# Kernel optimization log

Measured on AMD Instinct MI355X. Metric: run time of the kernel, lower is better.

Reference implementation:

```python
import jax, jax.numpy as jnp
import numpy as np

N = 50000          # nodes
E = 800000         # edges (COO)
IN_CH = 128
H1, H2, OUT = 200, 100, 2   # 100*out, 50*out, out with out_channels=2
EPS = 1e-12
DROP_P = 0.1


def setup_inputs() -> dict:
    key = jax.random.key(0)
    ks = jax.random.split(key, 6)
    x = jax.random.normal(ks[0], (N, IN_CH), dtype=jnp.float32)
    edge_index = jax.random.randint(ks[1], (2, E), 0, N)
    W1 = jax.random.normal(ks[2], (IN_CH, H1), dtype=jnp.float32) / np.sqrt(IN_CH)
    W2 = jax.random.normal(ks[3], (H1, H2), dtype=jnp.float32) / np.sqrt(H1)
    W3 = jax.random.normal(ks[4], (H2, OUT), dtype=jnp.float32) / np.sqrt(H2)
    beta1 = jnp.float32(1.0)
    beta2 = jnp.float32(1.0)
    beta3 = jnp.float32(1.0)
    return dict(x=x, edge_index=edge_index, W1=W1, W2=W2, W3=W3,
                beta1=beta1, beta2=beta2, beta3=beta3)


def _agnn_layer(x, W, beta, src, dst):
    # project in -> out channels, then AGNN cosine-attention propagation
    h = x @ W                                               # [N, D]
    hn = h / jnp.maximum(jnp.linalg.norm(h, axis=-1, keepdims=True), EPS)
    a = beta * jnp.sum(hn[src] * hn[dst], axis=-1)          # [E'] edge logits
    amax = jax.ops.segment_max(a, dst, num_segments=N)      # stable segment softmax
    amax = jnp.where(jnp.isfinite(amax), amax, 0.0)
    e = jnp.exp(a - amax[dst])
    denom = jax.ops.segment_sum(e, dst, num_segments=N)
    alpha = e / jnp.maximum(denom[dst], EPS)
    return jax.ops.segment_sum(h[src] * alpha[:, None], dst, num_segments=N)


def _dropout(k, x, p=DROP_P):
    keep = jax.random.bernoulli(k, 1.0 - p, x.shape)
    return jnp.where(keep, x / (1.0 - p), 0.0)


def reference(x, edge_index, W1, W2, W3, beta1, beta2, beta3):
    src, dst = edge_index[0], edge_index[1]
    loop = jnp.arange(N)                                    # self-loops (AGNNConv default)
    src = jnp.concatenate([src, loop])
    dst = jnp.concatenate([dst, loop])
    k1, k2 = jax.random.split(jax.random.key(42))
    h = jax.nn.relu(_agnn_layer(x, W1, beta1, src, dst))
    h = _dropout(k1, h)
    h = jax.nn.relu(_agnn_layer(h, W2, beta2, src, dst))
    h = _dropout(k2, h)
    h = jax.nn.relu(_agnn_layer(h, W3, beta3, src, dst))
    return h
```

## Files before the change

### kernel.cpp

```cpp
#include <hip/hip_runtime.h>
#include <hip/hip_bf16.h>

#define NN 50000
#define NE 800000
#define EPSN 1e-12f


#define H_OFF    0ull
#define A_OFF    40000000ull
#define H3_OFF   80000000ull
#define RINV_OFF 80400000ull
#define OFFS_OFF 80600000ull
#define DEG_OFF  80800016ull
#define CURS_OFF 81000016ull
#define ESRC_OFF 81200016ull
#define CHNK_OFF 84600016ull

__host__ __device__ inline void tf20(unsigned k0, unsigned k1, unsigned& x0, unsigned& x1) {
  unsigned ks2 = k0 ^ k1 ^ 0x1BD11BDAu;
  x0 += k0; x1 += k1;
#define TFR(r) { x0 += x1; x1 = ((x1 << (r)) | (x1 >> (32 - (r)))) ^ x0; }
  TFR(13) TFR(15) TFR(26) TFR(6)
  x0 += k1;  x1 += ks2 + 1u;
  TFR(17) TFR(29) TFR(16) TFR(24)
  x0 += ks2; x1 += k0 + 2u;
  TFR(13) TFR(15) TFR(26) TFR(6)
  x0 += k0;  x1 += k1 + 3u;
  TFR(17) TFR(29) TFR(16) TFR(24)
  x0 += k1;  x1 += ks2 + 4u;
  TFR(13) TFR(15) TFR(26) TFR(6)
  x0 += ks2; x1 += k0 + 5u;
#undef TFR
}

__device__ __forceinline__ float dropf(float val, unsigned k0, unsigned k1, unsigned i) {
  unsigned x0 = 0u, x1 = i;
  tf20(k0, k1, x0, x1);
  unsigned bits = x0 ^ x1;
  float u = __uint_as_float((bits >> 9) | 0x3F800000u) - 1.0f;
  return (u < 0.9f) ? val * (1.0f / 0.9f) : 0.0f;
}

__device__ __forceinline__ float wave_sum(float x) {
  x += __shfl_xor(x, 32); x += __shfl_xor(x, 16); x += __shfl_xor(x, 8);
  x += __shfl_xor(x, 4);  x += __shfl_xor(x, 2);  x += __shfl_xor(x, 1);
  return x;
}

template<int K, int KT, int NLP, int N>
__device__ __forceinline__ void gemm_core4(float* __restrict__ As, float* __restrict__ Ws,
                                           const float* __restrict__ A,
                                           const float* __restrict__ W,
                                           float* __restrict__ H,
                                           float* __restrict__ RINV, int M, int row0) {
  static_assert(NLP % 64 == 0 && KT % 4 == 0, "layout");
  constexpr int KTP = KT + 1, NV = N / 4, NC = NLP / 64, PD4 = NLP / 4 - NV;
  const float4* A4 = (const float4*)A;
  const float4* W4 = (const float4*)W;
  const float4* Ws4 = (const float4*)Ws;

  int t = threadIdx.x, rgrp = t >> 4, cg = t & 15;
  float acc[4][NC * 4];
#pragma unroll
  for (int rr = 0; rr < 4; rr++)
#pragma unroll
    for (int j = 0; j < NC * 4; j++) acc[rr][j] = 0.f;

  for (int k0 = 0; k0 < K; k0 += KT) {
    __syncthreads();
    for (int idx = t; idx < 64 * (KT / 4); idx += 256) {
      int r = idx / (KT / 4), cq = idx - r * (KT / 4);
      int gr = row0 + r;
      float4 v = (gr < M) ? A4[(size_t)gr * (K / 4) + (k0 / 4) + cq]
                          : make_float4(0.f, 0.f, 0.f, 0.f);
      float* dst = &As[r * KTP + cq * 4];
      dst[0] = v.x; dst[1] = v.y; dst[2] = v.z; dst[3] = v.w;
    }
    for (int idx = t; idx < KT * NV; idx += 256) {
      int kk = idx / NV, cq = idx - kk * NV;
      *(float4*)&Ws[kk * NLP + cq * 4] = W4[(size_t)(k0 + kk) * NV + cq];
    }
    for (int idx = t; idx < KT * PD4; idx += 256) {
      int kk = idx / PD4, pq = idx - kk * PD4;
      *(float4*)&Ws[kk * NLP + N + pq * 4] = make_float4(0.f, 0.f, 0.f, 0.f);
    }
    __syncthreads();
#pragma unroll
    for (int kk = 0; kk < KT; kk++) {
      float a[4];
#pragma unroll
      for (int rr = 0; rr < 4; rr++) a[rr] = As[(rgrp * 4 + rr) * KTP + kk];
#pragma unroll
      for (int q = 0; q < NC; q++) {
        float4 wv = Ws4[kk * (NLP / 4) + cg + 16 * q];
#pragma unroll
        for (int rr = 0; rr < 4; rr++) {
          acc[rr][q * 4 + 0] = fmaf(a[rr], wv.x, acc[rr][q * 4 + 0]);
          acc[rr][q * 4 + 1] = fmaf(a[rr], wv.y, acc[rr][q * 4 + 1]);
          acc[rr][q * 4 + 2] = fmaf(a[rr], wv.z, acc[rr][q * 4 + 2]);
          acc[rr][q * 4 + 3] = fmaf(a[rr], wv.w, acc[rr][q * 4 + 3]);
        }
      }
    }
  }

  int r0 = row0 + rgrp * 4;
#pragma unroll
  for (int rr = 0; rr < 4; rr++) {
    int gr = r0 + rr;
    float ss = 0.f;
#pragma unroll
    for (int q = 0; q < NC; q++) {
#pragma unroll
      for (int j = 0; j < 4; j++) {
        float v = acc[rr][q * 4 + j];
        ss += v * v;
        int c = 4 * (cg + 16 * q) + j;
        if (gr < M && c < N) H[(size_t)gr * N + c] = v;
      }
    }
    ss += __shfl_xor(ss, 1); ss += __shfl_xor(ss, 2);
    ss += __shfl_xor(ss, 4); ss += __shfl_xor(ss, 8);
    if (cg == 0 && gr < M) RINV[gr] = 1.0f / fmaxf(sqrtf(ss), EPSN);
  }
}

__global__ __launch_bounds__(256, 4) void gemm1_hist_kernel(
    const float* __restrict__ X, const float* __restrict__ W1,
    float* __restrict__ H, float* __restrict__ RINV,
    const int* __restrict__ EI, int* __restrict__ DEG) {
  __shared__ float As[64 * 17];
  __shared__ float Ws[16 * 256];
  int bid = blockIdx.x;
  if (bid < 782) {
    gemm_core4<128, 16, 256, 200>(As, Ws, X, W1, H, RINV, NN, bid * 64);
  } else {
    for (int e = (bid - 782) * 256 + threadIdx.x; e < NE; e += 242 * 256)
      atomicAdd(&DEG[EI[NE + e]], 1);
  }
}

__global__ __launch_bounds__(256, 4) void gemm2_kernel(const float* __restrict__ A,
                                                       const float* __restrict__ W,
                                                       float* __restrict__ H,
                                                       float* __restrict__ RINV, int M) {
  __shared__ float As[64 * 41];
  __shared__ float Ws[40 * 128];
  gemm_core4<200, 40, 128, 100>(As, Ws, A, W, H, RINV, M, blockIdx.x * 64);
}

__global__ __launch_bounds__(256) void csr_scan1_kernel(const int* __restrict__ deg,
                                                        int* __restrict__ offs,
                                                        int* __restrict__ chunk) {
  __shared__ int lds[8];
  int t = threadIdx.x;
  int base = blockIdx.x * 1024 + t * 4;
  int d[4];
#pragma unroll
  for (int j = 0; j < 4; j++) d[j] = (base + j < NN) ? deg[base + j] : 0;
  int ts = d[0] + d[1] + d[2] + d[3];
  int lane = t & 63, wave = t >> 6;
  int inc = ts;
#pragma unroll
  for (int sh = 1; sh < 64; sh <<= 1) { int u = __shfl_up(inc, sh); if (lane >= sh) inc += u; }
  if (lane == 63) lds[wave] = inc;
  __syncthreads();
  if (t == 0) { int s = 0; for (int w = 0; w < 4; w++) { int x = lds[w]; lds[w] = s; s += x; } lds[4] = s; }
  __syncthreads();
  int p = lds[wave] + inc - ts;
#pragma unroll
  for (int j = 0; j < 4; j++) { if (base + j < NN) offs[base + j] = p; p += d[j]; }
  if (t == 255) chunk[blockIdx.x] = lds[4];
}

__global__ __launch_bounds__(64) void csr_scan2_kernel(int* __restrict__ chunk) {
  int t = threadIdx.x;
  int v = (t < 49) ? chunk[t] : 0;
  int inc = v;
#pragma unroll
  for (int sh = 1; sh < 64; sh <<= 1) { int u = __shfl_up(inc, sh); if (t >= sh) inc += u; }
  if (t < 49) chunk[t] = inc - v;
}

__global__ __launch_bounds__(256) void csr_scan3_kernel(int* __restrict__ offs,
                                                        const int* __restrict__ chunk,
                                                        int* __restrict__ curs) {
  int i = blockIdx.x * 256 + threadIdx.x;
  if (i < NN) {
    int val = offs[i] + chunk[i >> 10];
    offs[i] = val;
    curs[i] = val;
  }
  if (i == 0) offs[NN] = NE;
}

__global__ __launch_bounds__(256) void csr_scatter_kernel(const int* __restrict__ ei,
                                                          int* __restrict__ curs,
                                                          int* __restrict__ esrc) {
  int e = blockIdx.x * 256 + threadIdx.x;
  if (e >= NE) return;
  int s = ei[e], d = ei[NE + e];
  int pos = atomicAdd(&curs[d], 1);
  esrc[pos] = s;
}

template<int D, int VEC, bool DROP>
__device__ __forceinline__ void attn_body(const float* __restrict__ H,
                                          const float* __restrict__ RINV,
                                          const int* __restrict__ OFFS,
                                          const int* __restrict__ ESRC,
                                          const float* __restrict__ BETA,
                                          float* __restrict__ OUT,
                                          unsigned k0, unsigned k1) {
  constexpr int NL = D / VEC;
  int v = blockIdx.x * 4 + (threadIdx.x >> 6);
  int lane = threadIdx.x & 63;
  bool act = lane < NL;
  float beta = BETA[0];
  float bd = beta * RINV[v];
  int e0 = OFFS[v], e1 = OFFS[v + 1];

  float wself = __expf(beta);
  float s = wself;
  float hd[VEC], acc[VEC];
  if (act) {
    const float* hrow = H + (size_t)v * D + lane * VEC;
    if (VEC == 4) { float4 tv = *(const float4*)hrow; hd[0] = tv.x; hd[1] = tv.y; hd[2] = tv.z; hd[3] = tv.w; }
    else          { float2 tv = *(const float2*)hrow; hd[0] = tv.x; hd[1] = tv.y; }
#pragma unroll
    for (int j = 0; j < VEC; j++) acc[j] = wself * hd[j];
  }

  int idx = e0;
  for (; idx + 4 <= e1; idx += 4) {
    int   u[4];
    float r[4], dt[4], hs[4][VEC];
#pragma unroll
    for (int m = 0; m < 4; m++) u[m] = ESRC[idx + m];
#pragma unroll
    for (int m = 0; m < 4; m++) r[m] = RINV[u[m]];
    float dd[4] = {0.f, 0.f, 0.f, 0.f};
    if (act) {
#pragma unroll
      for (int m = 0; m < 4; m++) {
        const float* p = H + (size_t)u[m] * D + lane * VEC;
        if (VEC == 4) { float4 a = *(const float4*)p; hs[m][0] = a.x; hs[m][1] = a.y; hs[m][2] = a.z; hs[m][3] = a.w; }
        else          { float2 a = *(const float2*)p; hs[m][0] = a.x; hs[m][1] = a.y; }
      }
#pragma unroll
      for (int m = 0; m < 4; m++)
#pragma unroll
        for (int j = 0; j < VEC; j++) dd[m] = fmaf(hd[j], hs[m][j], dd[m]);
    }
#pragma unroll
    for (int m = 0; m < 4; m++) dt[m] = wave_sum(dd[m]);
    float w[4];
#pragma unroll
    for (int m = 0; m < 4; m++) { w[m] = __expf(bd * dt[m] * r[m]); s += w[m]; }
    if (act) {
#pragma unroll
      for (int m = 0; m < 4; m++)
#pragma unroll
        for (int j = 0; j < VEC; j++) acc[j] = fmaf(w[m], hs[m][j], acc[j]);
    }
  }
  for (; idx < e1; ++idx) {
    int u0 = ESRC[idx];
    float r0 = RINV[u0];
    float h0[VEC];
    float ddt = 0.f;
    if (act) {
      const float* p0 = H + (size_t)u0 * D + lane * VEC;
      if (VEC == 4) { float4 a = *(const float4*)p0; h0[0] = a.x; h0[1] = a.y; h0[2] = a.z; h0[3] = a.w; }
      else          { float2 a = *(const float2*)p0; h0[0] = a.x; h0[1] = a.y; }
#pragma unroll
      for (int j = 0; j < VEC; j++) ddt = fmaf(hd[j], h0[j], ddt);
    }
    ddt = wave_sum(ddt);
    float w0 = __expf(bd * ddt * r0);
    s += w0;
    if (act) {
#pragma unroll
      for (int j = 0; j < VEC; j++) acc[j] = fmaf(w0, h0[j], acc[j]);
    }
  }

  float rs = 1.0f / fmaxf(s, EPSN);
  if (act) {
    float o[VEC];
#pragma unroll
    for (int j = 0; j < VEC; j++) {
      float val = acc[j] * rs;
      val = (val <= 0.0f) ? 0.0f : val;
      if (DROP) val = dropf(val, k0, k1, (unsigned)(v * D + lane * VEC + j));
      o[j] = val;
    }
    float* orow = OUT + (size_t)v * D + lane * VEC;
    if (VEC == 4) *(float4*)orow = make_float4(o[0], o[1], o[2], o[3]);
    else          *(float2*)orow = make_float2(o[0], o[1]);
  }
}

__global__ __launch_bounds__(256) void attn1_kernel(const float* H, const float* RINV,
                                                    const int* OFFS, const int* ESRC,
                                                    const float* BETA, float* OUT,
                                                    unsigned k0, unsigned k1) {
  attn_body<200, 4, true>(H, RINV, OFFS, ESRC, BETA, OUT, k0, k1);
}

__global__ __launch_bounds__(256) void attn2_proj_kernel(
    const float* __restrict__ H, const float* __restrict__ RINV,
    const int* __restrict__ OFFS, const int* __restrict__ ESRC,
    const float* __restrict__ BETA, const float* __restrict__ W3,
    float* __restrict__ H3, float* __restrict__ RINV3,
    unsigned k0, unsigned k1) {
  constexpr int D = 100, VEC = 2, NL = 50;
  int v = blockIdx.x * 4 + (threadIdx.x >> 6);
  int lane = threadIdx.x & 63;
  bool act = lane < NL;
  float beta = BETA[0];
  float bd = beta * RINV[v];
  int e0 = OFFS[v], e1 = OFFS[v + 1];

  float4 w3v = make_float4(0.f, 0.f, 0.f, 0.f);
  if (act) w3v = *(const float4*)&W3[4 * lane];

  float wself = __expf(beta);
  float s = wself;
  float hd[VEC], acc[VEC];
  if (act) {
    const float* hrow = H + (size_t)v * D + lane * VEC;
    float2 tv = *(const float2*)hrow; hd[0] = tv.x; hd[1] = tv.y;
#pragma unroll
    for (int j = 0; j < VEC; j++) acc[j] = wself * hd[j];
  }

  int idx = e0;
  for (; idx + 4 <= e1; idx += 4) {
    int   u[4];
    float r[4], dt[4], hs[4][VEC];
#pragma unroll
    for (int m = 0; m < 4; m++) u[m] = ESRC[idx + m];
#pragma unroll
    for (int m = 0; m < 4; m++) r[m] = RINV[u[m]];
    float dd[4] = {0.f, 0.f, 0.f, 0.f};
    if (act) {
#pragma unroll
      for (int m = 0; m < 4; m++) {
        const float* p = H + (size_t)u[m] * D + lane * VEC;
        float2 a = *(const float2*)p; hs[m][0] = a.x; hs[m][1] = a.y;
      }
#pragma unroll
      for (int m = 0; m < 4; m++)
#pragma unroll
        for (int j = 0; j < VEC; j++) dd[m] = fmaf(hd[j], hs[m][j], dd[m]);
    }
#pragma unroll
    for (int m = 0; m < 4; m++) dt[m] = wave_sum(dd[m]);
    float w[4];
#pragma unroll
    for (int m = 0; m < 4; m++) { w[m] = __expf(bd * dt[m] * r[m]); s += w[m]; }
    if (act) {
#pragma unroll
      for (int m = 0; m < 4; m++)
#pragma unroll
        for (int j = 0; j < VEC; j++) acc[j] = fmaf(w[m], hs[m][j], acc[j]);
    }
  }
  for (; idx < e1; ++idx) {
    int u0 = ESRC[idx];
    float r0 = RINV[u0];
    float h0[VEC];
    float ddt = 0.f;
    if (act) {
      const float* p0 = H + (size_t)u0 * D + lane * VEC;
      float2 a = *(const float2*)p0; h0[0] = a.x; h0[1] = a.y;
#pragma unroll
      for (int j = 0; j < VEC; j++) ddt = fmaf(hd[j], h0[j], ddt);
    }
    ddt = wave_sum(ddt);
    float w0 = __expf(bd * ddt * r0);
    s += w0;
    if (act) {
#pragma unroll
      for (int j = 0; j < VEC; j++) acc[j] = fmaf(w0, h0[j], acc[j]);
    }
  }

  float rs = 1.0f / fmaxf(s, EPSN);
  float p0 = 0.f, p1 = 0.f;
  if (act) {
    float o[VEC];
#pragma unroll
    for (int j = 0; j < VEC; j++) {
      float val = acc[j] * rs;
      val = (val <= 0.0f) ? 0.0f : val;
      val = dropf(val, k0, k1, (unsigned)(v * D + lane * VEC + j));
      o[j] = val;
    }
    p0 = o[0] * w3v.x + o[1] * w3v.z;
    p1 = o[0] * w3v.y + o[1] * w3v.w;
  }
  p0 = wave_sum(p0);
  p1 = wave_sum(p1);
  if (lane == 0) {
    H3[2 * v] = p0; H3[2 * v + 1] = p1;
    RINV3[v] = 1.0f / fmaxf(sqrtf(p0 * p0 + p1 * p1), EPSN);
  }
}

__global__ __launch_bounds__(256) void attn3_kernel(const float* __restrict__ H3,
                                                    const float* __restrict__ RINV3,
                                                    const int* __restrict__ OFFS,
                                                    const int* __restrict__ ESRC,
                                                    const float* __restrict__ BETA,
                                                    float* __restrict__ out) {
  int v = blockIdx.x * 4 + (threadIdx.x >> 6);
  int lane = threadIdx.x & 63;
  float beta = BETA[0];
  float bd = beta * RINV3[v];
  float h0 = H3[2 * v], h1 = H3[2 * v + 1];
  int e0 = OFFS[v], e1 = OFFS[v + 1];
  float s = 0.f, a0 = 0.f, a1 = 0.f;
  for (int idx = e0 + lane; idx < e1; idx += 64) {
    int u = ESRC[idx];
    float s0 = H3[2 * u], s1 = H3[2 * u + 1];
    float w = __expf(bd * (h0 * s0 + h1 * s1) * RINV3[u]);
    s += w; a0 = fmaf(w, s0, a0); a1 = fmaf(w, s1, a1);
  }
  s = wave_sum(s); a0 = wave_sum(a0); a1 = wave_sum(a1);
  if (lane == 0) {
    float wself = __expf(beta);
    s += wself; a0 = fmaf(wself, h0, a0); a1 = fmaf(wself, h1, a1);
    float rs = 1.0f / fmaxf(s, EPSN);
    float o0 = a0 * rs, o1 = a1 * rs;
    out[2 * v]     = (o0 <= 0.0f) ? 0.0f : o0;
    out[2 * v + 1] = (o1 <= 0.0f) ? 0.0f : o1;
  }
}

extern "C" void kernel_launch(void* const* d_in, const int* in_sizes, int n_in,
                              void* d_out, int out_size, void* d_ws, size_t ws_size,
                              hipStream_t stream) {
  const float* X  = (const float*)d_in[0];
  const int*   EI = (const int*)d_in[1];
  const float* W1 = (const float*)d_in[2];
  const float* W2 = (const float*)d_in[3];
  const float* W3 = (const float*)d_in[4];
  const float* B1 = (const float*)d_in[5];
  const float* B2 = (const float*)d_in[6];
  const float* B3 = (const float*)d_in[7];

  char* ws = (char*)d_ws;
  float* H     = (float*)(ws + H_OFF);
  float* A     = (float*)(ws + A_OFF);
  float* H3    = (float*)(ws + H3_OFF);
  float* RINV  = (float*)(ws + RINV_OFF);
  int* OFFS    = (int*)(ws + OFFS_OFF);
  int* DEG     = (int*)(ws + DEG_OFF);
  int* CURS    = (int*)(ws + CURS_OFF);
  float* RINV3 = (float*)(ws + CURS_OFF);
  int* ESRC    = (int*)(ws + ESRC_OFF);
  int* CHNK    = (int*)(ws + CHNK_OFF);

  unsigned k1a = 0u, k1b = 0u; tf20(0u, 42u, k1a, k1b);
  unsigned k2a = 0u, k2b = 1u; tf20(0u, 42u, k2a, k2b);

  hipMemsetAsync(DEG, 0, NN * sizeof(int), stream);

  gemm1_hist_kernel<<<1024, 256, 0, stream>>>(X, W1, H, RINV, EI, DEG);
  csr_scan1_kernel<<<49, 256, 0, stream>>>(DEG, OFFS, CHNK);
  csr_scan2_kernel<<<1, 64, 0, stream>>>(CHNK);
  csr_scan3_kernel<<<196, 256, 0, stream>>>(OFFS, CHNK, CURS);
  csr_scatter_kernel<<<(NE + 255) / 256, 256, 0, stream>>>(EI, CURS, ESRC);

  const int gb = (NN + 63) / 64;
  const int ab = NN / 4;

  attn1_kernel<<<ab, 256, 0, stream>>>(H, RINV, OFFS, ESRC, B1, A, k1a, k1b);
  gemm2_kernel<<<gb, 256, 0, stream>>>(A, W2, H, RINV, NN);
  attn2_proj_kernel<<<ab, 256, 0, stream>>>(H, RINV, OFFS, ESRC, B2, W3, H3, RINV3, k2a, k2b);
  attn3_kernel<<<ab, 256, 0, stream>>>(H3, RINV3, OFFS, ESRC, B3, (float*)d_out);
}
```

Before: 464.7 us.

## Schedule attention waves over nodes sorted by descending in-degree

Adds a counting sort of nodes by in-degree (histogram, scan, scatter into a permutation), and the three attention kernels now take their node through this permutation. High-degree nodes run first, which is meant to cut load imbalance and the long tail of waves. The inner loops also drop the per-lane active predicate and instead zero-fill inactive lanes. This costs three small extra kernels and a memset, and block-level locality between neighbouring node ids is lost.

New measurement: 751.7 us. +61.8%, slower.

```diff
diff --git a/kernel.cpp b/kernel.cpp
--- a/kernel.cpp
+++ b/kernel.cpp
@@ -14,6 +14,7 @@
 #define DEG_OFF  80800016ull
 #define CURS_OFF 81000016ull
 #define ESRC_OFF 81200016ull
+#define VPRM_OFF 84400016ull
 #define CHNK_OFF 84600016ull
 
 __host__ __device__ inline void tf20(unsigned k0, unsigned k1, unsigned& x0, unsigned& x1) {
@@ -204,32 +205,73 @@
   esrc[pos] = s;
 }
 
+__global__ __launch_bounds__(256) void perm_hist_kernel(const int* __restrict__ deg,
+                                                        int* __restrict__ pbkt) {
+  int v = blockIdx.x * 256 + threadIdx.x;
+  if (v >= NN) return;
+  int b = 511 - min(deg[v], 511);
+  atomicAdd(&pbkt[b], 1);
+}
+
+__global__ __launch_bounds__(256) void perm_scan_kernel(const int* __restrict__ pbkt,
+                                                        int* __restrict__ pcur) {
+  __shared__ int lds[8];
+  int t = threadIdx.x;
+  int b0 = pbkt[2 * t], b1 = pbkt[2 * t + 1];
+  int ts = b0 + b1;
+  int lane = t & 63, wave = t >> 6;
+  int inc = ts;
+#pragma unroll
+  for (int sh = 1; sh < 64; sh <<= 1) { int u = __shfl_up(inc, sh); if (lane >= sh) inc += u; }
+  if (lane == 63) lds[wave] = inc;
+  __syncthreads();
+  if (t == 0) { int s = 0; for (int w = 0; w < 4; w++) { int x = lds[w]; lds[w] = s; s += x; } }
+  __syncthreads();
+  int p = lds[wave] + inc - ts;
+  pcur[2 * t] = p;
+  pcur[2 * t + 1] = p + b0;
+}
+
+__global__ __launch_bounds__(256) void perm_scat_kernel(const int* __restrict__ deg,
+                                                        int* __restrict__ pcur,
+                                                        int* __restrict__ vperm) {
+  int v = blockIdx.x * 256 + threadIdx.x;
+  if (v >= NN) return;
+  int b = 511 - min(deg[v], 511);
+  int pos = atomicAdd(&pcur[b], 1);
+  vperm[pos] = v;
+}
+
 template<int D, int VEC, bool DROP>
 __device__ __forceinline__ void attn_body(const float* __restrict__ H,
                                           const float* __restrict__ RINV,
                                           const int* __restrict__ OFFS,
                                           const int* __restrict__ ESRC,
+                                          const int* __restrict__ VPERM,
                                           const float* __restrict__ BETA,
                                           float* __restrict__ OUT,
                                           unsigned k0, unsigned k1) {
   constexpr int NL = D / VEC;
-  int v = blockIdx.x * 4 + (threadIdx.x >> 6);
+  int v = VPERM[blockIdx.x * 4 + (threadIdx.x >> 6)];
   int lane = threadIdx.x & 63;
   bool act = lane < NL;
+  const float* hrow = H + (size_t)v * D + lane * VEC;
+  float hd[VEC];
+#pragma unroll
+  for (int j = 0; j < VEC; j++) hd[j] = 0.f;
+  if (act) {
+    if (VEC == 4) { float4 tv = *(const float4*)hrow; hd[0] = tv.x; hd[1] = tv.y; hd[2] = tv.z; hd[3] = tv.w; }
+    else          { float2 tv = *(const float2*)hrow; hd[0] = tv.x; hd[1] = tv.y; }
+  }
   float beta = BETA[0];
   float bd = beta * RINV[v];
   int e0 = OFFS[v], e1 = OFFS[v + 1];
 
   float wself = __expf(beta);
   float s = wself;
-  float hd[VEC], acc[VEC];
-  if (act) {
-    const float* hrow = H + (size_t)v * D + lane * VEC;
-    if (VEC == 4) { float4 tv = *(const float4*)hrow; hd[0] = tv.x; hd[1] = tv.y; hd[2] = tv.z; hd[3] = tv.w; }
-    else          { float2 tv = *(const float2*)hrow; hd[0] = tv.x; hd[1] = tv.y; }
-#pragma unroll
-    for (int j = 0; j < VEC; j++) acc[j] = wself * hd[j];
-  }
+  float acc[VEC];
+#pragma unroll
+  for (int j = 0; j < VEC; j++) acc[j] = wself * hd[j];
 
   int idx = e0;
   for (; idx + 4 <= e1; idx += 4) {
@@ -239,50 +281,50 @@
     for (int m = 0; m < 4; m++) u[m] = ESRC[idx + m];
 #pragma unroll
     for (int m = 0; m < 4; m++) r[m] = RINV[u[m]];
-    float dd[4] = {0.f, 0.f, 0.f, 0.f};
-    if (act) {
-#pragma unroll
-      for (int m = 0; m < 4; m++) {
-        const float* p = H + (size_t)u[m] * D + lane * VEC;
+#pragma unroll
+    for (int m = 0; m < 4; m++) {
+      const float* p = H + (size_t)u[m] * D + lane * VEC;
+#pragma unroll
+      for (int j = 0; j < VEC; j++) hs[m][j] = 0.f;
+      if (act) {
         if (VEC == 4) { float4 a = *(const float4*)p; hs[m][0] = a.x; hs[m][1] = a.y; hs[m][2] = a.z; hs[m][3] = a.w; }
         else          { float2 a = *(const float2*)p; hs[m][0] = a.x; hs[m][1] = a.y; }
       }
-#pragma unroll
-      for (int m = 0; m < 4; m++)
-#pragma unroll
-        for (int j = 0; j < VEC; j++) dd[m] = fmaf(hd[j], hs[m][j], dd[m]);
-    }
-#pragma unroll
-    for (int m = 0; m < 4; m++) dt[m] = wave_sum(dd[m]);
-    float w[4];
-#pragma unroll
-    for (int m = 0; m < 4; m++) { w[m] = __expf(bd * dt[m] * r[m]); s += w[m]; }
-    if (act) {
-#pragma unroll
-      for (int m = 0; m < 4; m++)
-#pragma unroll
-        for (int j = 0; j < VEC; j++) acc[j] = fmaf(w[m], hs[m][j], acc[j]);
+    }
+#pragma unroll
+    for (int m = 0; m < 4; m++) {
+      float d = 0.f;
+#pragma unroll
+      for (int j = 0; j < VEC; j++) d = fmaf(hd[j], hs[m][j], d);
+      dt[m] = wave_sum(d);
+    }
+#pragma unroll
+    for (int m = 0; m < 4; m++) {
+      float w = __expf(bd * dt[m] * r[m]);
+      s += w;
+#pragma unroll
+      for (int j = 0; j < VEC; j++) acc[j] = fmaf(w, hs[m][j], acc[j]);
     }
   }
   for (; idx < e1; ++idx) {
     int u0 = ESRC[idx];
     float r0 = RINV[u0];
+    const float* p0 = H + (size_t)u0 * D + lane * VEC;
     float h0[VEC];
-    float ddt = 0.f;
+#pragma unroll
+    for (int j = 0; j < VEC; j++) h0[j] = 0.f;
     if (act) {
-      const float* p0 = H + (size_t)u0 * D + lane * VEC;
       if (VEC == 4) { float4 a = *(const float4*)p0; h0[0] = a.x; h0[1] = a.y; h0[2] = a.z; h0[3] = a.w; }
       else          { float2 a = *(const float2*)p0; h0[0] = a.x; h0[1] = a.y; }
-#pragma unroll
-      for (int j = 0; j < VEC; j++) ddt = fmaf(hd[j], h0[j], ddt);
-    }
-    ddt = wave_sum(ddt);
-    float w0 = __expf(bd * ddt * r0);
+    }
+    float d0 = 0.f;
+#pragma unroll
+    for (int j = 0; j < VEC; j++) d0 = fmaf(hd[j], h0[j], d0);
+    d0 = wave_sum(d0);
+    float w0 = __expf(bd * d0 * r0);
     s += w0;
-    if (act) {
-#pragma unroll
-      for (int j = 0; j < VEC; j++) acc[j] = fmaf(w0, h0[j], acc[j]);
-    }
+#pragma unroll
+    for (int j = 0; j < VEC; j++) acc[j] = fmaf(w0, h0[j], acc[j]);
   }
 
   float rs = 1.0f / fmaxf(s, EPSN);
@@ -303,37 +345,39 @@
 
 __global__ __launch_bounds__(256) void attn1_kernel(const float* H, const float* RINV,
                                                     const int* OFFS, const int* ESRC,
+                                                    const int* VPERM,
                                                     const float* BETA, float* OUT,
                                                     unsigned k0, unsigned k1) {
-  attn_body<200, 4, true>(H, RINV, OFFS, ESRC, BETA, OUT, k0, k1);
+  attn_body<200, 4, true>(H, RINV, OFFS, ESRC, VPERM, BETA, OUT, k0, k1);
 }
 
 __global__ __launch_bounds__(256) void attn2_proj_kernel(
     const float* __restrict__ H, const float* __restrict__ RINV,
     const int* __restrict__ OFFS, const int* __restrict__ ESRC,
+    const int* __restrict__ VPERM,
     const float* __restrict__ BETA, const float* __restrict__ W3,
     float* __restrict__ H3, float* __restrict__ RINV3,
     unsigned k0, unsigned k1) {
   constexpr int D = 100, VEC = 2, NL = 50;
-  int v = blockIdx.x * 4 + (threadIdx.x >> 6);
+  int v = VPERM[blockIdx.x * 4 + (threadIdx.x >> 6)];
   int lane = threadIdx.x & 63;
   bool act = lane < NL;
+  const float* hrow = H + (size_t)v * D + lane * VEC;
+  float hd[VEC];
+  hd[0] = 0.f; hd[1] = 0.f;
+  float4 w3v = make_float4(0.f, 0.f, 0.f, 0.f);
+  if (act) {
+    float2 tv = *(const float2*)hrow; hd[0] = tv.x; hd[1] = tv.y;
+    w3v = *(const float4*)&W3[4 * lane];
+  }
   float beta = BETA[0];
   float bd = beta * RINV[v];
   int e0 = OFFS[v], e1 = OFFS[v + 1];
 
-  float4 w3v = make_float4(0.f, 0.f, 0.f, 0.f);
-  if (act) w3v = *(const float4*)&W3[4 * lane];
-
   float wself = __expf(beta);
   float s = wself;
-  float hd[VEC], acc[VEC];
-  if (act) {
-    const float* hrow = H + (size_t)v * D + lane * VEC;
-    float2 tv = *(const float2*)hrow; hd[0] = tv.x; hd[1] = tv.y;
-#pragma unroll
-    for (int j = 0; j < VEC; j++) acc[j] = wself * hd[j];
-  }
+  float acc[VEC];
+  acc[0] = wself * hd[0]; acc[1] = wself * hd[1];
 
   int idx = e0;
   for (; idx + 4 <= e1; idx += 4) {
@@ -343,63 +387,54 @@
     for (int m = 0; m < 4; m++) u[m] = ESRC[idx + m];
 #pragma unroll
     for (int m = 0; m < 4; m++) r[m] = RINV[u[m]];
-    float dd[4] = {0.f, 0.f, 0.f, 0.f};
-    if (act) {
-#pragma unroll
-      for (int m = 0; m < 4; m++) {
-        const float* p = H + (size_t)u[m] * D + lane * VEC;
-        float2 a = *(const float2*)p; hs[m][0] = a.x; hs[m][1] = a.y;
-      }
-#pragma unroll
-      for (int m = 0; m < 4; m++)
-#pragma unroll
-        for (int j = 0; j < VEC; j++) dd[m] = fmaf(hd[j], hs[m][j], dd[m]);
-    }
-#pragma unroll
-    for (int m = 0; m < 4; m++) dt[m] = wave_sum(dd[m]);
-    float w[4];
-#pragma unroll
-    for (int m = 0; m < 4; m++) { w[m] = __expf(bd * dt[m] * r[m]); s += w[m]; }
-    if (act) {
-#pragma unroll
-      for (int m = 0; m < 4; m++)
-#pragma unroll
-        for (int j = 0; j < VEC; j++) acc[j] = fmaf(w[m], hs[m][j], acc[j]);
+#pragma unroll
+    for (int m = 0; m < 4; m++) {
+      const float* p = H + (size_t)u[m] * D + lane * VEC;
+      hs[m][0] = 0.f; hs[m][1] = 0.f;
+      if (act) { float2 a = *(const float2*)p; hs[m][0] = a.x; hs[m][1] = a.y; }
+    }
+#pragma unroll
+    for (int m = 0; m < 4; m++) {
+      float d = 0.f;
+#pragma unroll
+      for (int j = 0; j < VEC; j++) d = fmaf(hd[j], hs[m][j], d);
+      dt[m] = wave_sum(d);
+    }
+#pragma unroll
+    for (int m = 0; m < 4; m++) {
+      float w = __expf(bd * dt[m] * r[m]);
+      s += w;
+#pragma unroll
+      for (int j = 0; j < VEC; j++) acc[j] = fmaf(w, hs[m][j], acc[j]);
     }
   }
   for (; idx < e1; ++idx) {
     int u0 = ESRC[idx];
     float r0 = RINV[u0];
+    const float* p0 = H + (size_t)u0 * D + lane * VEC;
     float h0[VEC];
-    float ddt = 0.f;
-    if (act) {
-      const float* p0 = H + (size_t)u0 * D + lane * VEC;
-      float2 a = *(const float2*)p0; h0[0] = a.x; h0[1] = a.y;
-#pragma unroll
-      for (int j = 0; j < VEC; j++) ddt = fmaf(hd[j], h0[j], ddt);
-    }
-    ddt = wave_sum(ddt);
-    float w0 = __expf(bd * ddt * r0);
+    h0[0] = 0.f; h0[1] = 0.f;
+    if (act) { float2 a = *(const float2*)p0; h0[0] = a.x; h0[1] = a.y; }
+    float d0 = 0.f;
+#pragma unroll
+    for (int j = 0; j < VEC; j++) d0 = fmaf(hd[j], h0[j], d0);
+    d0 = wave_sum(d0);
+    float w0 = __expf(bd * d0 * r0);
     s += w0;
-    if (act) {
-#pragma unroll
-      for (int j = 0; j < VEC; j++) acc[j] = fmaf(w0, h0[j], acc[j]);
-    }
+#pragma unroll
+    for (int j = 0; j < VEC; j++) acc[j] = fmaf(w0, h0[j], acc[j]);
   }
 
   float rs = 1.0f / fmaxf(s, EPSN);
   float p0 = 0.f, p1 = 0.f;
   if (act) {
-    float o[VEC];
-#pragma unroll
-    for (int j = 0; j < VEC; j++) {
-      float val = acc[j] * rs;
-      val = (val <= 0.0f) ? 0.0f : val;
-      val = dropf(val, k0, k1, (unsigned)(v * D + lane * VEC + j));
-      o[j] = val;
-    }
-    p0 = o[0] * w3v.x + o[1] * w3v.z;
-    p1 = o[0] * w3v.y + o[1] * w3v.w;
+    float o0 = acc[0] * rs, o1 = acc[1] * rs;
+    o0 = (o0 <= 0.0f) ? 0.0f : o0;
+    o1 = (o1 <= 0.0f) ? 0.0f : o1;
+    o0 = dropf(o0, k0, k1, (unsigned)(v * D + lane * VEC));
+    o1 = dropf(o1, k0, k1, (unsigned)(v * D + lane * VEC + 1));
+    p0 = o0 * w3v.x + o1 * w3v.z;
+    p1 = o0 * w3v.y + o1 * w3v.w;
   }
   p0 = wave_sum(p0);
   p1 = wave_sum(p1);
@@ -413,9 +448,10 @@
                                                     const float* __restrict__ RINV3,
                                                     const int* __restrict__ OFFS,
                                                     const int* __restrict__ ESRC,
+                                                    const int* __restrict__ VPERM,
                                                     const float* __restrict__ BETA,
                                                     float* __restrict__ out) {
-  int v = blockIdx.x * 4 + (threadIdx.x >> 6);
+  int v = VPERM[blockIdx.x * 4 + (threadIdx.x >> 6)];
   int lane = threadIdx.x & 63;
   float beta = BETA[0];
   float bd = beta * RINV3[v];
@@ -459,8 +495,11 @@
   int* OFFS    = (int*)(ws + OFFS_OFF);
   int* DEG     = (int*)(ws + DEG_OFF);
   int* CURS    = (int*)(ws + CURS_OFF);
+  int* PBKT    = (int*)(ws + CURS_OFF);
+  int* PCUR    = (int*)(ws + CURS_OFF + 2048);
   float* RINV3 = (float*)(ws + CURS_OFF);
   int* ESRC    = (int*)(ws + ESRC_OFF);
+  int* VPERM   = (int*)(ws + VPRM_OFF);
   int* CHNK    = (int*)(ws + CHNK_OFF);
 
   unsigned k1a = 0u, k1b = 0u; tf20(0u, 42u, k1a, k1b);
@@ -474,11 +513,16 @@
   csr_scan3_kernel<<<196, 256, 0, stream>>>(OFFS, CHNK, CURS);
   csr_scatter_kernel<<<(NE + 255) / 256, 256, 0, stream>>>(EI, CURS, ESRC);
 
+  hipMemsetAsync(PBKT, 0, 2048, stream);
+  perm_hist_kernel<<<196, 256, 0, stream>>>(DEG, PBKT);
+  perm_scan_kernel<<<1, 256, 0, stream>>>(PBKT, PCUR);
+  perm_scat_kernel<<<196, 256, 0, stream>>>(DEG, PCUR, VPERM);
+
   const int gb = (NN + 63) / 64;
   const int ab = NN / 4;
 
-  attn1_kernel<<<ab, 256, 0, stream>>>(H, RINV, OFFS, ESRC, B1, A, k1a, k1b);
+  attn1_kernel<<<ab, 256, 0, stream>>>(H, RINV, OFFS, ESRC, VPERM, B1, A, k1a, k1b);
   gemm2_kernel<<<gb, 256, 0, stream>>>(A, W2, H, RINV, NN);
-  attn2_proj_kernel<<<ab, 256, 0, stream>>>(H, RINV, OFFS, ESRC, B2, W3, H3, RINV3, k2a, k2b);
-  attn3_kernel<<<ab, 256, 0, stream>>>(H3, RINV3, OFFS, ESRC, B3, (float*)d_out);
-}
+  attn2_proj_kernel<<<ab, 256, 0, stream>>>(H, RINV, OFFS, ESRC, VPERM, B2, W3, H3, RINV3, k2a, k2b);
+  attn3_kernel<<<ab, 256, 0, stream>>>(H3, RINV3, OFFS, ESRC, VPERM, B3, (float*)d_out);
+}
```
